# Performance work log

Hardware: AMD Instinct MI355X
Metric: run time of the kernel (lower is better)

The kernel has to match this reference:

```python
import jax, jax.numpy as jnp
import numpy as np

R0 = 1.0
DIM_A, DIM_V, DIM_D = 32, 32, 32
N_NODES = 20000
N_EDGES = 640000


def radial_encode_8(r, r0):
    # 8 Gaussian radial basis functions on the edge length |r_ij|
    d = jnp.linalg.norm(r, axis=-1)                      # [E]
    centers = jnp.linspace(0.0, r0, 8)                   # [8]
    width = r0 / 8.0
    return jnp.exp(-(((d[..., None] - centers) / width) ** 2))  # [E,8]


def tens_sigmoid_vec(v):
    # norm-saturating nonlinearity for rank-1 tensors (direction-preserving)
    n2 = jnp.sum(v * v, axis=-1, keepdims=True)
    return v * jax.lax.rsqrt(1.0 + n2)


def setup_inputs() -> dict:
    key = jax.random.key(0)
    ks = jax.random.split(key, 12)

    def lin(k, fan_in, fan_out):
        return jax.random.normal(k, (fan_in, fan_out), jnp.float32) / np.float32(np.sqrt(fan_in))

    return dict(
        r_ij=jax.random.normal(ks[0], (N_EDGES, 3), jnp.float32),
        w_rad=lin(ks[1], 8, DIM_A), b_rad=jnp.zeros((DIM_A,), jnp.float32),
        w_direct=lin(ks[2], DIM_A, DIM_A),
        w1=lin(ks[3], DIM_A, 2 * DIM_A), b1=jnp.zeros((2 * DIM_A,), jnp.float32),
        w2=lin(ks[4], 2 * DIM_A, 2 * DIM_A), b2=jnp.zeros((2 * DIM_A,), jnp.float32),
        w3=lin(ks[5], 2 * DIM_A, DIM_A), b3=jnp.zeros((DIM_A,), jnp.float32),
        w_v=lin(ks[6], DIM_A, DIM_V),
        w_d=lin(ks[7], DIM_A, DIM_D),
        edges_src=jax.random.randint(ks[8], (N_EDGES,), 0, N_NODES),
        n_nodes=N_NODES,
    )


def reference(r_ij, w_rad, b_rad, w_direct, w1, b1, w2, b2, w3, b3, w_v, w_d,
              edges_src, n_nodes):
    lrelu = lambda x: jnp.where(x > 0, x, 0.1 * x)
    # radial MLP: Linear(8, a) -> MLP (lin_direct + 3-layer leakyrelu net)
    h = radial_encode_8(r_ij, R0) @ w_rad + b_rad                      # [E,a]
    rad = h @ w_direct + (lrelu(lrelu(h @ w1 + b1) @ w2 + b2) @ w3 + b3)  # [E,a]
    rs = tens_sigmoid_vec(r_ij * (7.0 / R0))                            # [E,3]

    seg = lambda x: jax.ops.segment_sum(x, edges_src, num_segments=n_nodes)
    A_a = seg(rad)                                                      # [N,a]
    A_v = seg(rad[:, :, None] * rs[:, None, :])                         # [N,a,3]
    # phi_d_ij = rad ⊗ rs ⊗ rs per edge  -> [E,a,3,3], then scatter-sum
    A_d = seg(rad[:, :, None, None] * rs[:, None, None, :] * rs[:, None, :, None])  # [N,a,3,3]

    out_v = jnp.einsum('nac,av->nvc', A_v, w_v)                         # TensLinear rank 1
    out_d = jnp.einsum('naij,ad->ndij', A_d, w_d)                       # TensLinear rank 2
    return A_a, out_v, out_d
```

## Files before the change

kernel.cpp:

```cpp
#include <hip/hip_runtime.h>
#include <hip/hip_bf16.h>
#include <hip/hip_fp16.h>
#include <math.h>


#define TSIZE 8192
#define DMAX  2.0f
#define EPB   4
#define HB    128
#define TILE  10240
#define NPB   4

#define O_WRAD 0
#define O_BRAD 256
#define O_WDIR 288
#define O_W1   1312
#define O_B1   3360
#define O_W2   3424
#define O_B2   7520
#define O_W3   7584
#define O_B3   9632
#define O_WV   9664
#define O_WD   10688
#define W_TOT  11712

__device__ __forceinline__ float lrelu(float x) { return x > 0.0f ? x : 0.1f * x; }

__device__ __forceinline__ float ldf(const void* p, int i, bool f32) {
    return f32 ? ((const float*)p)[i]
               : __uint_as_float(((unsigned int)((const unsigned short*)p)[i]) << 16);
}
__device__ __forceinline__ void stf(void* p, size_t i, float v, bool f32) {
    if (f32) ((float*)p)[i] = v;
    else     ((__hip_bfloat16*)p)[i] = __float2bfloat16(v);
}

__device__ __forceinline__ bool detect_f32(const void* r) {
    const unsigned short* p = (const unsigned short*)r;
    int bad = 0;
#pragma unroll 8
    for (int i = 0; i < 128; i++) {
        float v = __uint_as_float(((unsigned int)p[i]) << 16);
        bad |= (!isfinite(v) || fabsf(v) > 1e5f) ? 1 : 0;
    }
    return bad != 0;
}

__global__ void k_prep(const void* __restrict__ r_ij,
                       const void* w_rad, const void* b_rad, const void* w_direct,
                       const void* w1, const void* b1, const void* w2, const void* b2,
                       const void* w3, const void* b3, const void* w_v, const void* w_d,
                       float* __restrict__ wcat, int* __restrict__ flag,
                       int* __restrict__ counts, int N) {
    const int b = blockIdx.x;
    if (b == 0) {
        if (threadIdx.x == 0) flag[0] = detect_f32(r_ij) ? 1 : 0;
    } else if (b <= 11) {
        const bool f32 = detect_f32(r_ij);
        const void* src; int cnt; int off;
        switch (b) {
            case 1:  src = w_rad;    cnt = 256;  off = O_WRAD; break;
            case 2:  src = b_rad;    cnt = 32;   off = O_BRAD; break;
            case 3:  src = w_direct; cnt = 1024; off = O_WDIR; break;
            case 4:  src = w1;       cnt = 2048; off = O_W1;   break;
            case 5:  src = b1;       cnt = 64;   off = O_B1;   break;
            case 6:  src = w2;       cnt = 4096; off = O_W2;   break;
            case 7:  src = b2;       cnt = 64;   off = O_B2;   break;
            case 8:  src = w3;       cnt = 2048; off = O_W3;   break;
            case 9:  src = b3;       cnt = 32;   off = O_B3;   break;
            case 10: src = w_v;      cnt = 1024; off = O_WV;   break;
            default: src = w_d;      cnt = 1024; off = O_WD;   break;
        }
        for (int i = threadIdx.x; i < cnt; i += blockDim.x)
            wcat[off + i] = ldf(src, i, f32);
    } else if (counts) {
        int i = (b - 12) * blockDim.x + threadIdx.x;
        if (i < N) counts[i] = 0;
    }
}

__global__ void __launch_bounds__(64 * EPB) k_table(const float* __restrict__ wcat,
                                                    float* __restrict__ tabI) {
    __shared__ float Lh[EPB][32], Lt1[EPB][64], Lt2[EPB][64], Lrad[EPB][32];

    const int s = threadIdx.x >> 6;
    const int j = threadIdx.x & 63;
    const int e = blockIdx.x * EPB + s;
    const float d = (float)e * (DMAX / (float)(TSIZE - 1));

    float enc[8];
#pragma unroll
    for (int k = 0; k < 8; k++) {
        float t = (d - (float)k * (1.0f / 7.0f)) * 8.0f;
        enc[k] = expf(-t * t);
    }

    if (j < 32) {
        float hv = wcat[O_BRAD + j];
#pragma unroll
        for (int k = 0; k < 8; k++) hv = fmaf(enc[k], wcat[O_WRAD + k * 32 + j], hv);
        Lh[s][j] = hv;
    }
    __syncthreads();

    {
        float v = wcat[O_B1 + j];
#pragma unroll
        for (int i = 0; i < 32; i++) v = fmaf(Lh[s][i], wcat[O_W1 + i * 64 + j], v);
        Lt1[s][j] = lrelu(v);
    }
    __syncthreads();

    {
        float v = wcat[O_B2 + j];
#pragma unroll
        for (int i = 0; i < 64; i++) v = fmaf(Lt1[s][i], wcat[O_W2 + i * 64 + j], v);
        Lt2[s][j] = lrelu(v);
    }
    __syncthreads();

    if (j < 32) {
        float v = wcat[O_B3 + j];
#pragma unroll
        for (int i = 0; i < 64; i++) v = fmaf(Lt2[s][i], wcat[O_W3 + i * 32 + j], v);
#pragma unroll
        for (int i = 0; i < 32; i++) v = fmaf(Lh[s][i], wcat[O_WDIR + i * 32 + j], v);
        Lrad[s][j] = v;
        tabI[e * 96 + j] = v;
    }
    __syncthreads();

    if (j < 32) {
        float sv = 0.0f, sd = 0.0f;
#pragma unroll
        for (int i = 0; i < 32; i++) {
            float ri = Lrad[s][i];
            sv = fmaf(ri, wcat[O_WV + i * 32 + j], sv);
            sd = fmaf(ri, wcat[O_WD + i * 32 + j], sd);
        }
        tabI[e * 96 + 32 + j] = sv;
        tabI[e * 96 + 64 + j] = sd;
    }
}

__global__ void __launch_bounds__(256) k_hist(const int* __restrict__ src, int E,
                                              int chunk,
                                              unsigned short* __restrict__ cnt,
                                              int N) {
    __shared__ int lcnt[TILE];
    const int b = blockIdx.x % HB;
    const int t = blockIdx.x / HB;
    const int lo = b * chunk;
    const int hi = min(lo + chunk, E);
    const int t0 = t * TILE;
    const int tl = min(TILE, N - t0);

    for (int i = threadIdx.x; i < tl; i += 256) lcnt[i] = 0;
    __syncthreads();
    for (int e = lo + threadIdx.x; e < hi; e += 256) {
        const int s = src[e] - t0;
        if ((unsigned)s < (unsigned)tl) atomicAdd(&lcnt[s], 1);
    }
    __syncthreads();
    unsigned short* out = cnt + (size_t)(t * HB + b) * TILE;
    for (int i = threadIdx.x; i < tl; i += 256)
        out[i] = (unsigned short)lcnt[i];
}

__global__ void __launch_bounds__(64) k_colscan(unsigned short* __restrict__ cnt,
                                                int* __restrict__ tot,
                                                int* __restrict__ coarse, int N) {
    const int lane = threadIdx.x;
    const int n = blockIdx.x * 64 + lane;
    int run = 0;
    if (n < N) {
        const int t = n / TILE;
        const int nl = n % TILE;
        unsigned short* col = cnt + (size_t)(t * HB) * TILE + nl;
#pragma unroll 4
        for (int b = 0; b < HB; b++) {
            int c = col[(size_t)b * TILE];
            col[(size_t)b * TILE] = (unsigned short)run;
            run += c;
        }
        tot[n] = run;
    }
    int s = run;
    for (int off = 32; off > 0; off >>= 1) s += __shfl_down(s, off);
    if (lane == 0) coarse[blockIdx.x] = s;
}

__global__ void __launch_bounds__(64) k_scan2(const int* __restrict__ tot,
                                              const int* __restrict__ coarse,
                                              int* __restrict__ rowstart, int N) {
    const int lane = threadIdx.x;
    const int b = blockIdx.x;
    int cp = 0;
    for (int j = lane; j < b; j += 64) cp += coarse[j];
    for (int off = 32; off > 0; off >>= 1) cp += __shfl_down(cp, off);
    const int cpre = __shfl(cp, 0);

    const int n = b * 64 + lane;
    const int v = (n < N) ? tot[n] : 0;
    int inc = v;
    for (int off = 1; off < 64; off <<= 1) {
        int y = __shfl_up(inc, off);
        if (lane >= off) inc += y;
    }
    if (n < N) rowstart[n] = cpre + inc - v;
    if (n == N - 1) rowstart[N] = cpre + inc;
}

template <bool P16>
__global__ void __launch_bounds__(256) k_place(
        const int* __restrict__ src, int E, int chunk,
        const unsigned short* __restrict__ cnt, const int* __restrict__ rowstart,
        const void* __restrict__ r_ij, const int* __restrict__ flag,
        void* __restrict__ epsv, int N) {
    __shared__ int cur[TILE];
    const int b = blockIdx.x % HB;
    const int t = blockIdx.x / HB;
    const int lo = b * chunk;
    const int hi = min(lo + chunk, E);
    const int t0 = t * TILE;
    const int tl = min(TILE, N - t0);
    const bool f32 = flag[0] != 0;

    const unsigned short* base = cnt + (size_t)(t * HB + b) * TILE;
    for (int i = threadIdx.x; i < tl; i += 256)
        cur[i] = rowstart[t0 + i] + (int)base[i];
    __syncthreads();
    for (int e = lo + threadIdx.x; e < hi; e += 256) {
        const int s = src[e] - t0;
        if ((unsigned)s < (unsigned)tl) {
            const int pos = atomicAdd(&cur[s], 1);
            const float x = ldf(r_ij, 3 * e + 0, f32);
            const float y = ldf(r_ij, 3 * e + 1, f32);
            const float z = ldf(r_ij, 3 * e + 2, f32);
            const float d2 = x * x + y * y + z * z;
            const float inv = rsqrtf(1.0f + 49.0f * d2);
            const float u = fminf(sqrtf(d2), DMAX) * ((float)(TSIZE - 1) / DMAX);
            const int ti = (int)(u + 0.5f);
            const float rs0 = 7.0f * x * inv, rs1 = 7.0f * y * inv,
                        rs2 = 7.0f * z * inv;
            if (P16) {
                ((float4*)epsv)[pos] =
                    make_float4(rs0, rs1, rs2, __int_as_float(ti * 384));
            } else {
                const unsigned int h0 = __half_as_ushort(__float2half(rs0));
                const unsigned int h1 = __half_as_ushort(__float2half(rs1));
                const unsigned int h2 = __half_as_ushort(__float2half(rs2));
                ((uint2*)epsv)[pos] =
                    make_uint2(h0 | (h1 << 16), h2 | ((unsigned)ti << 16));
            }
        }
    }
}

template <bool P16>
__global__ void __launch_bounds__(64 * NPB) k_nodes2(
    const void* __restrict__ epsv,
    const int* __restrict__ rowstart,
    const float* __restrict__ tabI,
    const int* __restrict__ flag,
    void* __restrict__ out, int N) {
    const int wave = threadIdx.x >> 6;
    const int lane = threadIdx.x & 63;
    const int n0 = (blockIdx.x * NPB + wave) * 2;
    const int a = lane & 31;
    const int half = lane >> 5;
    const int myn = n0 + half;
    const bool f32 = flag[0] != 0;
    const char* tabA = (const char*)tabI + (a << 2);

    int s0 = 0, s1 = 0;
    if (myn < N) { s0 = rowstart[myn]; s1 = rowstart[myn + 1]; }
    const int mylen = s1 - s0;
    const int lenA = __shfl(mylen, 0);
    const int lenB = __shfl(mylen, 32);
    const int minl = min(lenA, lenB);
    const int maxl = max(lenA, lenB);

    float accA = 0.f, v0 = 0.f, v1 = 0.f, v2 = 0.f;
    float d00 = 0.f, d01 = 0.f, d02 = 0.f,
          d10 = 0.f, d11 = 0.f, d12 = 0.f,
          d20 = 0.f, d21 = 0.f, d22 = 0.f;

#define EDGE_ACC(X, Y, Z, P)                                                  \
    do {                                                                      \
        const float ra = (P)[0], rv = (P)[32], rd = (P)[64];                  \
        accA += ra;                                                           \
        v0 += rv * (X); v1 += rv * (Y); v2 += rv * (Z);                       \
        const float t0 = rd * (X), t1 = rd * (Y), t2 = rd * (Z);              \
        d00 += t0 * (X); d01 += t0 * (Y); d02 += t0 * (Z);                    \
        d10 += t1 * (X); d11 += t1 * (Y); d12 += t1 * (Z);                    \
        d20 += t2 * (X); d21 += t2 * (Y); d22 += t2 * (Z);                    \
    } while (0)

    int i = 0;
    for (; i + 1 < minl; i += 2) {
        float x0, y0, z0, x1, y1, z1;
        const float *p0, *p1;
        if (P16) {
            const float4 qa = ((const float4*)epsv)[s0 + i];
            const float4 qb = ((const float4*)epsv)[s0 + i + 1];
            x0 = qa.x; y0 = qa.y; z0 = qa.z;
            x1 = qb.x; y1 = qb.y; z1 = qb.z;
            p0 = (const float*)(tabA + __float_as_int(qa.w));
            p1 = (const float*)(tabA + __float_as_int(qb.w));
        } else {
            const uint2 qa = ((const uint2*)epsv)[s0 + i];
            const uint2 qb = ((const uint2*)epsv)[s0 + i + 1];
            x0 = __half2float(__ushort_as_half((unsigned short)(qa.x & 0xffff)));
            y0 = __half2float(__ushort_as_half((unsigned short)(qa.x >> 16)));
            z0 = __half2float(__ushort_as_half((unsigned short)(qa.y & 0xffff)));
            x1 = __half2float(__ushort_as_half((unsigned short)(qb.x & 0xffff)));
            y1 = __half2float(__ushort_as_half((unsigned short)(qb.x >> 16)));
            z1 = __half2float(__ushort_as_half((unsigned short)(qb.y & 0xffff)));
            p0 = (const float*)(tabA + (int)(qa.y >> 16) * 384);
            p1 = (const float*)(tabA + (int)(qb.y >> 16) * 384);
        }
        EDGE_ACC(x0, y0, z0, p0);
        EDGE_ACC(x1, y1, z1, p1);
    }
    for (; i < maxl; i++) {
        if (i < mylen) {
            float x, y, z;
            const float* p;
            if (P16) {
                const float4 q = ((const float4*)epsv)[s0 + i];
                x = q.x; y = q.y; z = q.z;
                p = (const float*)(tabA + __float_as_int(q.w));
            } else {
                const uint2 q = ((const uint2*)epsv)[s0 + i];
                x = __half2float(__ushort_as_half((unsigned short)(q.x & 0xffff)));
                y = __half2float(__ushort_as_half((unsigned short)(q.x >> 16)));
                z = __half2float(__ushort_as_half((unsigned short)(q.y & 0xffff)));
                p = (const float*)(tabA + (int)(q.y >> 16) * 384);
            }
            EDGE_ACC(x, y, z, p);
        }
    }
#undef EDGE_ACC

    if (myn >= N) return;
    const size_t baseV = (size_t)N * 32;
    const size_t baseD = (size_t)N * 128;
    stf(out, (size_t)myn * 32 + a, accA, f32);
    const size_t vb = baseV + (size_t)myn * 96 + a * 3;
    stf(out, vb + 0, v0, f32);
    stf(out, vb + 1, v1, f32);
    stf(out, vb + 2, v2, f32);
    const size_t db = baseD + (size_t)myn * 288 + a * 9;
    stf(out, db + 0, d00, f32);
    stf(out, db + 1, d01, f32);
    stf(out, db + 2, d02, f32);
    stf(out, db + 3, d10, f32);
    stf(out, db + 4, d11, f32);
    stf(out, db + 5, d12, f32);
    stf(out, db + 6, d20, f32);
    stf(out, db + 7, d21, f32);
    stf(out, db + 8, d22, f32);
}

__global__ void k_rank_g(const int* __restrict__ src, int* __restrict__ counts,
                         int* __restrict__ rank, int E) {
    int e = blockIdx.x * blockDim.x + threadIdx.x;
    if (e < E) rank[e] = atomicAdd(&counts[src[e]], 1);
}
__global__ void k_scan_g(const int* __restrict__ counts, int* __restrict__ rowstart,
                         int N, int E) {
    __shared__ int part[1024];
    const int t = threadIdx.x;
    const int CH = (N + 1023) / 1024;
    const int lo = t * CH;
    const int hi = min(lo + CH, N);
    int s = 0;
    for (int i = lo; i < hi; i++) s += counts[i];
    part[t] = s;
    __syncthreads();
    for (int off = 1; off < 1024; off <<= 1) {
        int v = part[t];
        int w = (t >= off) ? part[t - off] : 0;
        __syncthreads();
        part[t] = v + w;
        __syncthreads();
    }
    int run = (t == 0) ? 0 : part[t - 1];
    for (int i = lo; i < hi; i++) { rowstart[i] = run; run += counts[i]; }
    if (t == 0) rowstart[N] = E;
}
__global__ void k_place_g(const int* __restrict__ src, const int* __restrict__ rank,
                          const int* __restrict__ rowstart,
                          int* __restrict__ perm, int E) {
    int e = blockIdx.x * blockDim.x + threadIdx.x;
    if (e < E) perm[rowstart[src[e]] + rank[e]] = e;
}
__global__ void __launch_bounds__(256) k_nodes_fb(
    const int* __restrict__ perm, const void* __restrict__ r_ij,
    const int* __restrict__ rowstart, const float* __restrict__ tabI,
    const int* __restrict__ flag, void* __restrict__ out, int N) {
    const int wave = threadIdx.x >> 6;
    const int lane = threadIdx.x & 63;
    const int n = blockIdx.x * 4 + wave;
    if (n >= N) return;
    const int a = lane & 31;
    const bool hi = (lane >> 5) != 0;
    const bool f32 = flag[0] != 0;
    const int s0 = rowstart[n], s1 = rowstart[n + 1];
    float accR = 0.f, acc1 = 0.f, acc2 = 0.f, acc3 = 0.f,
          acc4 = 0.f, acc5 = 0.f, acc6 = 0.f;
    for (int idx = s0; idx < s1; idx++) {
        const int e = perm[idx];
        const float x0 = ldf(r_ij, 3 * e + 0, f32);
        const float y0 = ldf(r_ij, 3 * e + 1, f32);
        const float z0 = ldf(r_ij, 3 * e + 2, f32);
        const float d2 = x0 * x0 + y0 * y0 + z0 * z0;
        const float inv = rsqrtf(1.0f + 49.0f * d2);
        const float x = 7.0f * x0 * inv, y = 7.0f * y0 * inv, z = 7.0f * z0 * inv;
        const float u = fminf(sqrtf(d2), DMAX) * ((float)(TSIZE - 1) / DMAX);
        const int b = (int)(u + 0.5f) * 96 + a;
        const float ra = tabI[b], rv = tabI[b + 32], rd = tabI[b + 64];
        const float b1 = (hi ? rd : rv) * (hi ? y : 1.0f);
        const float b2 = rd * (hi ? z : x);
        accR += ra;
        acc1 += b1 * x; acc2 += b1 * y; acc3 += b1 * z;
        acc4 += b2 * x; acc5 += b2 * y; acc6 += b2 * z;
    }
    const size_t baseV = (size_t)N * 32;
    const size_t baseD = (size_t)N * 128;
    if (!hi) {
        stf(out, (size_t)n * 32 + a, accR, f32);
        const size_t vb = baseV + (size_t)n * 96 + a * 3;
        stf(out, vb + 0, acc1, f32);
        stf(out, vb + 1, acc2, f32);
        stf(out, vb + 2, acc3, f32);
        const size_t db = baseD + (size_t)n * 288 + a * 9;
        stf(out, db + 0, acc4, f32);
        stf(out, db + 1, acc5, f32);
        stf(out, db + 2, acc6, f32);
    } else {
        const size_t db = baseD + (size_t)n * 288 + a * 9;
        stf(out, db + 3, acc1, f32);
        stf(out, db + 4, acc2, f32);
        stf(out, db + 5, acc3, f32);
        stf(out, db + 6, acc4, f32);
        stf(out, db + 7, acc5, f32);
        stf(out, db + 8, acc6, f32);
    }
}

extern "C" void kernel_launch(void* const* d_in, const int* in_sizes, int n_in,
                              void* d_out, int out_size, void* d_ws, size_t ws_size,
                              hipStream_t stream) {
    const void* r_ij     = d_in[0];
    const void* w_rad    = d_in[1];
    const void* b_rad    = d_in[2];
    const void* w_direct = d_in[3];
    const void* w1       = d_in[4];
    const void* b1       = d_in[5];
    const void* w2       = d_in[6];
    const void* b2       = d_in[7];
    const void* w3       = d_in[8];
    const void* b3       = d_in[9];
    const void* w_v      = d_in[10];
    const void* w_d      = d_in[11];
    const int* edges_src = (const int*)d_in[12];

    const int E = in_sizes[12];
    const int N = out_size / 416;
    const int chunk = (E + HB - 1) / HB;
    const int ntiles = (N + TILE - 1) / TILE;
    const int NB = (N + 63) / 64;

    const size_t cntBytes  = (size_t)ntiles * HB * TILE * 2;
    const size_t tailBytes = ((size_t)W_TOT + 4) * 4 + (size_t)TSIZE * 96 * 4
                           + cntBytes + ((size_t)N + NB + N + 1) * 4;
    const bool p16 = ws_size >= (size_t)E * 16 + tailBytes + 64;
    const bool p8  = !p16 && ws_size >= (size_t)E * 8 + tailBytes + 64;

    char* w = (char*)d_ws;
    if (p16 || p8) {
        const size_t slot = (size_t)E * (p16 ? 16 : 8);
        void* eps     = (void*)w;
        float* wcat   = (float*)(w + slot);
        int* flag     = (int*)(wcat + W_TOT);
        float* tabI   = (float*)(flag + 4);
        unsigned short* cnt = (unsigned short*)(tabI + (size_t)TSIZE * 96);
        int* tot      = (int*)((char*)cnt + cntBytes);
        int* coarse   = tot + N;
        int* rowstart = coarse + NB;

        const int nodeBlocks = (N + 2 * NPB - 1) / (2 * NPB);
        k_prep<<<12, 256, 0, stream>>>(
            r_ij, w_rad, b_rad, w_direct, w1, b1, w2, b2, w3, b3, w_v, w_d,
            wcat, flag, nullptr, N);
        k_table<<<TSIZE / EPB, 64 * EPB, 0, stream>>>(wcat, tabI);
        k_hist<<<HB * ntiles, 256, 0, stream>>>(edges_src, E, chunk, cnt, N);
        k_colscan<<<NB, 64, 0, stream>>>(cnt, tot, coarse, N);
        k_scan2<<<NB, 64, 0, stream>>>(tot, coarse, rowstart, N);
        if (p16) {
            k_place<true><<<HB * ntiles, 256, 0, stream>>>(
                edges_src, E, chunk, cnt, rowstart, r_ij, flag, eps, N);
            k_nodes2<true><<<nodeBlocks, 64 * NPB, 0, stream>>>(
                eps, rowstart, tabI, flag, d_out, N);
        } else {
            k_place<false><<<HB * ntiles, 256, 0, stream>>>(
                edges_src, E, chunk, cnt, rowstart, r_ij, flag, eps, N);
            k_nodes2<false><<<nodeBlocks, 64 * NPB, 0, stream>>>(
                eps, rowstart, tabI, flag, d_out, N);
        }
    } else {
        int* perm     = (int*)w;
        float* wcat   = (float*)(w + (size_t)E * 4);
        int* flag     = (int*)(wcat + W_TOT);
        float* tabI   = (float*)(flag + 4);
        int* counts   = (int*)(tabI + (size_t)TSIZE * 96);
        int* rowstart = counts + N;
        int* rank     = rowstart + N + 1;

        k_prep<<<12 + (N + 255) / 256, 256, 0, stream>>>(
            r_ij, w_rad, b_rad, w_direct, w1, b1, w2, b2, w3, b3, w_v, w_d,
            wcat, flag, counts, N);
        k_table<<<TSIZE / EPB, 64 * EPB, 0, stream>>>(wcat, tabI);
        k_rank_g<<<(E + 255) / 256, 256, 0, stream>>>(edges_src, counts, rank, E);
        k_scan_g<<<1, 1024, 0, stream>>>(counts, rowstart, N, E);
        k_place_g<<<(E + 255) / 256, 256, 0, stream>>>(edges_src, rank, rowstart,
                                                       perm, E);
        k_nodes_fb<<<(N + 3) / 4, 256, 0, stream>>>(
            perm, r_ij, rowstart, tabI, flag, d_out, N);
    }
}
```

Before: 207.7 us.

## Fuse CSR build into one grid-barrier kernel and stage weights in shared memory

Merges the histogram, column scan, coarse scan and placement kernels into one persistent kernel that uses atomic-counter grid barriers, which removes several launch gaps. Folds the weight-conversion prep kernel into the table kernel, where each block loads all weights into shared memory. Also unrolls the node edge loop from 2 to 4 edges per iteration. The spin grid barrier assumes every block is co-resident (256 blocks of 256 threads with about 40KB of shared memory each) and adds a memset launch. Each table block now redundantly loads about 47KB of weights.

```diff
diff --git a/kernel.cpp b/kernel.cpp
--- a/kernel.cpp
+++ b/kernel.cpp
@@ -46,42 +46,37 @@
     return bad != 0;
 }
 
-__global__ void k_prep(const void* __restrict__ r_ij,
-                       const void* w_rad, const void* b_rad, const void* w_direct,
-                       const void* w1, const void* b1, const void* w2, const void* b2,
-                       const void* w3, const void* b3, const void* w_v, const void* w_d,
-                       float* __restrict__ wcat, int* __restrict__ flag,
-                       int* __restrict__ counts, int N) {
-    const int b = blockIdx.x;
-    if (b == 0) {
-        if (threadIdx.x == 0) flag[0] = detect_f32(r_ij) ? 1 : 0;
-    } else if (b <= 11) {
-        const bool f32 = detect_f32(r_ij);
-        const void* src; int cnt; int off;
-        switch (b) {
-            case 1:  src = w_rad;    cnt = 256;  off = O_WRAD; break;
-            case 2:  src = b_rad;    cnt = 32;   off = O_BRAD; break;
-            case 3:  src = w_direct; cnt = 1024; off = O_WDIR; break;
-            case 4:  src = w1;       cnt = 2048; off = O_W1;   break;
-            case 5:  src = b1;       cnt = 64;   off = O_B1;   break;
-            case 6:  src = w2;       cnt = 4096; off = O_W2;   break;
-            case 7:  src = b2;       cnt = 64;   off = O_B2;   break;
-            case 8:  src = w3;       cnt = 2048; off = O_W3;   break;
-            case 9:  src = b3;       cnt = 32;   off = O_B3;   break;
-            case 10: src = w_v;      cnt = 1024; off = O_WV;   break;
-            default: src = w_d;      cnt = 1024; off = O_WD;   break;
-        }
-        for (int i = threadIdx.x; i < cnt; i += blockDim.x)
-            wcat[off + i] = ldf(src, i, f32);
-    } else if (counts) {
-        int i = (b - 12) * blockDim.x + threadIdx.x;
-        if (i < N) counts[i] = 0;
-    }
-}
-
-__global__ void __launch_bounds__(64 * EPB) k_table(const float* __restrict__ wcat,
-                                                    float* __restrict__ tabI) {
+__device__ __forceinline__ void load_seg(float* dst, const void* src, int cnt,
+                                         bool f32, int tid, int bs) {
+    for (int i = tid; i < cnt; i += bs) dst[i] = ldf(src, i, f32);
+}
+
+__global__ void __launch_bounds__(64 * EPB) k_table(
+        const void* __restrict__ r_ij,
+        const void* w_rad, const void* b_rad, const void* w_direct,
+        const void* w1, const void* b1, const void* w2, const void* b2,
+        const void* w3, const void* b3, const void* w_v, const void* w_d,
+        int* __restrict__ flag, float* __restrict__ tabI) {
+    __shared__ float W[W_TOT];
     __shared__ float Lh[EPB][32], Lt1[EPB][64], Lt2[EPB][64], Lrad[EPB][32];
+
+    const bool f32 = detect_f32(r_ij);
+    if (blockIdx.x == 0 && threadIdx.x == 0) flag[0] = f32 ? 1 : 0;
+
+    const int tid = threadIdx.x;
+    const int bs = 64 * EPB;
+    load_seg(W + O_WRAD, w_rad,    256,  f32, tid, bs);
+    load_seg(W + O_BRAD, b_rad,    32,   f32, tid, bs);
+    load_seg(W + O_WDIR, w_direct, 1024, f32, tid, bs);
+    load_seg(W + O_W1,   w1,       2048, f32, tid, bs);
+    load_seg(W + O_B1,   b1,       64,   f32, tid, bs);
+    load_seg(W + O_W2,   w2,       4096, f32, tid, bs);
+    load_seg(W + O_B2,   b2,       64,   f32, tid, bs);
+    load_seg(W + O_W3,   w3,       2048, f32, tid, bs);
+    load_seg(W + O_B3,   b3,       32,   f32, tid, bs);
+    load_seg(W + O_WV,   w_v,      1024, f32, tid, bs);
+    load_seg(W + O_WD,   w_d,      1024, f32, tid, bs);
+    __syncthreads();
 
     const int s = threadIdx.x >> 6;
     const int j = threadIdx.x & 63;
@@ -96,35 +91,35 @@
     }
 
     if (j < 32) {
-        float hv = wcat[O_BRAD + j];
-#pragma unroll
-        for (int k = 0; k < 8; k++) hv = fmaf(enc[k], wcat[O_WRAD + k * 32 + j], hv);
+        float hv = W[O_BRAD + j];
+#pragma unroll
+        for (int k = 0; k < 8; k++) hv = fmaf(enc[k], W[O_WRAD + k * 32 + j], hv);
         Lh[s][j] = hv;
     }
     __syncthreads();
 
     {
-        float v = wcat[O_B1 + j];
-#pragma unroll
-        for (int i = 0; i < 32; i++) v = fmaf(Lh[s][i], wcat[O_W1 + i * 64 + j], v);
+        float v = W[O_B1 + j];
+#pragma unroll
+        for (int i = 0; i < 32; i++) v = fmaf(Lh[s][i], W[O_W1 + i * 64 + j], v);
         Lt1[s][j] = lrelu(v);
     }
     __syncthreads();
 
     {
-        float v = wcat[O_B2 + j];
-#pragma unroll
-        for (int i = 0; i < 64; i++) v = fmaf(Lt1[s][i], wcat[O_W2 + i * 64 + j], v);
+        float v = W[O_B2 + j];
+#pragma unroll
+        for (int i = 0; i < 64; i++) v = fmaf(Lt1[s][i], W[O_W2 + i * 64 + j], v);
         Lt2[s][j] = lrelu(v);
     }
     __syncthreads();
 
     if (j < 32) {
-        float v = wcat[O_B3 + j];
-#pragma unroll
-        for (int i = 0; i < 64; i++) v = fmaf(Lt2[s][i], wcat[O_W3 + i * 32 + j], v);
-#pragma unroll
-        for (int i = 0; i < 32; i++) v = fmaf(Lh[s][i], wcat[O_WDIR + i * 32 + j], v);
+        float v = W[O_B3 + j];
+#pragma unroll
+        for (int i = 0; i < 64; i++) v = fmaf(Lt2[s][i], W[O_W3 + i * 32 + j], v);
+#pragma unroll
+        for (int i = 0; i < 32; i++) v = fmaf(Lh[s][i], W[O_WDIR + i * 32 + j], v);
         Lrad[s][j] = v;
         tabI[e * 96 + j] = v;
     }
@@ -135,19 +130,34 @@
 #pragma unroll
         for (int i = 0; i < 32; i++) {
             float ri = Lrad[s][i];
-            sv = fmaf(ri, wcat[O_WV + i * 32 + j], sv);
-            sd = fmaf(ri, wcat[O_WD + i * 32 + j], sd);
+            sv = fmaf(ri, W[O_WV + i * 32 + j], sv);
+            sd = fmaf(ri, W[O_WD + i * 32 + j], sd);
         }
         tabI[e * 96 + 32 + j] = sv;
         tabI[e * 96 + 64 + j] = sd;
     }
 }
 
-__global__ void __launch_bounds__(256) k_hist(const int* __restrict__ src, int E,
-                                              int chunk,
-                                              unsigned short* __restrict__ cnt,
-                                              int N) {
-    __shared__ int lcnt[TILE];
+__device__ __forceinline__ void gbar(int* bar, int slot, int nb) {
+    __syncthreads();
+    if (threadIdx.x == 0) {
+        __threadfence();
+        atomicAdd(&bar[slot], 1);
+        while (atomicAdd(&bar[slot], 0) < nb) { }
+    }
+    __syncthreads();
+    __threadfence();
+}
+
+template <bool P16>
+__global__ void __launch_bounds__(256) k_csr(
+        const int* __restrict__ src, int E, int chunk,
+        const void* __restrict__ r_ij, const int* __restrict__ flag,
+        unsigned short* __restrict__ cnt, int* __restrict__ tot,
+        int* __restrict__ coarse, int* __restrict__ rowstart,
+        int* __restrict__ bar, void* __restrict__ epsv, int N) {
+    __shared__ int lbuf[TILE];
+    const int nb = gridDim.x;
     const int b = blockIdx.x % HB;
     const int t = blockIdx.x / HB;
     const int lo = b * chunk;
@@ -155,103 +165,91 @@
     const int t0 = t * TILE;
     const int tl = min(TILE, N - t0);
 
-    for (int i = threadIdx.x; i < tl; i += 256) lcnt[i] = 0;
+    for (int i = threadIdx.x; i < tl; i += 256) lbuf[i] = 0;
     __syncthreads();
     for (int e = lo + threadIdx.x; e < hi; e += 256) {
         const int s = src[e] - t0;
-        if ((unsigned)s < (unsigned)tl) atomicAdd(&lcnt[s], 1);
-    }
-    __syncthreads();
-    unsigned short* out = cnt + (size_t)(t * HB + b) * TILE;
-    for (int i = threadIdx.x; i < tl; i += 256)
-        out[i] = (unsigned short)lcnt[i];
-}
-
-__global__ void __launch_bounds__(64) k_colscan(unsigned short* __restrict__ cnt,
-                                                int* __restrict__ tot,
-                                                int* __restrict__ coarse, int N) {
-    const int lane = threadIdx.x;
-    const int n = blockIdx.x * 64 + lane;
-    int run = 0;
-    if (n < N) {
-        const int t = n / TILE;
-        const int nl = n % TILE;
-        unsigned short* col = cnt + (size_t)(t * HB) * TILE + nl;
+        if ((unsigned)s < (unsigned)tl) atomicAdd(&lbuf[s], 1);
+    }
+    __syncthreads();
+    {
+        unsigned short* out = cnt + (size_t)(t * HB + b) * TILE;
+        for (int i = threadIdx.x; i < tl; i += 256)
+            out[i] = (unsigned short)lbuf[i];
+    }
+    gbar(bar, 0, nb);
+
+    {
+        const int gtid = blockIdx.x * 256 + threadIdx.x;
+        const int lane = threadIdx.x & 63;
+        const int w = gtid >> 6;
+        int run = 0;
+        if (gtid < N) {
+            const int tt = gtid / TILE;
+            const int nl = gtid % TILE;
+            unsigned short* col = cnt + (size_t)(tt * HB) * TILE + nl;
 #pragma unroll 4
-        for (int b = 0; b < HB; b++) {
-            int c = col[(size_t)b * TILE];
-            col[(size_t)b * TILE] = (unsigned short)run;
-            run += c;
+            for (int c = 0; c < HB; c++) {
+                int v = col[(size_t)c * TILE];
+                col[(size_t)c * TILE] = (unsigned short)run;
+                run += v;
+            }
+            tot[gtid] = run;
         }
-        tot[n] = run;
-    }
-    int s = run;
-    for (int off = 32; off > 0; off >>= 1) s += __shfl_down(s, off);
-    if (lane == 0) coarse[blockIdx.x] = s;
-}
-
-__global__ void __launch_bounds__(64) k_scan2(const int* __restrict__ tot,
-                                              const int* __restrict__ coarse,
-                                              int* __restrict__ rowstart, int N) {
-    const int lane = threadIdx.x;
-    const int b = blockIdx.x;
-    int cp = 0;
-    for (int j = lane; j < b; j += 64) cp += coarse[j];
-    for (int off = 32; off > 0; off >>= 1) cp += __shfl_down(cp, off);
-    const int cpre = __shfl(cp, 0);
-
-    const int n = b * 64 + lane;
-    const int v = (n < N) ? tot[n] : 0;
-    int inc = v;
-    for (int off = 1; off < 64; off <<= 1) {
-        int y = __shfl_up(inc, off);
-        if (lane >= off) inc += y;
-    }
-    if (n < N) rowstart[n] = cpre + inc - v;
-    if (n == N - 1) rowstart[N] = cpre + inc;
-}
-
-template <bool P16>
-__global__ void __launch_bounds__(256) k_place(
-        const int* __restrict__ src, int E, int chunk,
-        const unsigned short* __restrict__ cnt, const int* __restrict__ rowstart,
-        const void* __restrict__ r_ij, const int* __restrict__ flag,
-        void* __restrict__ epsv, int N) {
-    __shared__ int cur[TILE];
-    const int b = blockIdx.x % HB;
-    const int t = blockIdx.x / HB;
-    const int lo = b * chunk;
-    const int hi = min(lo + chunk, E);
-    const int t0 = t * TILE;
-    const int tl = min(TILE, N - t0);
-    const bool f32 = flag[0] != 0;
-
-    const unsigned short* base = cnt + (size_t)(t * HB + b) * TILE;
-    for (int i = threadIdx.x; i < tl; i += 256)
-        cur[i] = rowstart[t0 + i] + (int)base[i];
-    __syncthreads();
-    for (int e = lo + threadIdx.x; e < hi; e += 256) {
-        const int s = src[e] - t0;
-        if ((unsigned)s < (unsigned)tl) {
-            const int pos = atomicAdd(&cur[s], 1);
-            const float x = ldf(r_ij, 3 * e + 0, f32);
-            const float y = ldf(r_ij, 3 * e + 1, f32);
-            const float z = ldf(r_ij, 3 * e + 2, f32);
-            const float d2 = x * x + y * y + z * z;
-            const float inv = rsqrtf(1.0f + 49.0f * d2);
-            const float u = fminf(sqrtf(d2), DMAX) * ((float)(TSIZE - 1) / DMAX);
-            const int ti = (int)(u + 0.5f);
-            const float rs0 = 7.0f * x * inv, rs1 = 7.0f * y * inv,
-                        rs2 = 7.0f * z * inv;
-            if (P16) {
-                ((float4*)epsv)[pos] =
-                    make_float4(rs0, rs1, rs2, __int_as_float(ti * 384));
-            } else {
-                const unsigned int h0 = __half_as_ushort(__float2half(rs0));
-                const unsigned int h1 = __half_as_ushort(__float2half(rs1));
-                const unsigned int h2 = __half_as_ushort(__float2half(rs2));
-                ((uint2*)epsv)[pos] =
-                    make_uint2(h0 | (h1 << 16), h2 | ((unsigned)ti << 16));
+        int sum = run;
+        for (int off = 32; off > 0; off >>= 1) sum += __shfl_down(sum, off);
+        if (lane == 0) coarse[w] = sum;
+    }
+    gbar(bar, 1, nb);
+
+    {
+        const int gtid = blockIdx.x * 256 + threadIdx.x;
+        const int lane = threadIdx.x & 63;
+        const int w = gtid >> 6;
+        int cp = 0;
+        for (int j = lane; j < w; j += 64) cp += coarse[j];
+        for (int off = 32; off > 0; off >>= 1) cp += __shfl_down(cp, off);
+        const int cpre = __shfl(cp, 0);
+        const int v = (gtid < N) ? tot[gtid] : 0;
+        int inc = v;
+        for (int off = 1; off < 64; off <<= 1) {
+            int y = __shfl_up(inc, off);
+            if (lane >= off) inc += y;
+        }
+        if (gtid < N) rowstart[gtid] = cpre + inc - v;
+        if (gtid == N - 1) rowstart[N] = cpre + inc;
+    }
+    gbar(bar, 2, nb);
+
+    {
+        const bool f32 = flag[0] != 0;
+        const unsigned short* base = cnt + (size_t)(t * HB + b) * TILE;
+        for (int i = threadIdx.x; i < tl; i += 256)
+            lbuf[i] = rowstart[t0 + i] + (int)base[i];
+        __syncthreads();
+        for (int e = lo + threadIdx.x; e < hi; e += 256) {
+            const int s = src[e] - t0;
+            if ((unsigned)s < (unsigned)tl) {
+                const int pos = atomicAdd(&lbuf[s], 1);
+                const float x = ldf(r_ij, 3 * e + 0, f32);
+                const float y = ldf(r_ij, 3 * e + 1, f32);
+                const float z = ldf(r_ij, 3 * e + 2, f32);
+                const float d2 = x * x + y * y + z * z;
+                const float inv = rsqrtf(1.0f + 49.0f * d2);
+                const float u = fminf(sqrtf(d2), DMAX) * ((float)(TSIZE - 1) / DMAX);
+                const int ti = (int)(u + 0.5f);
+                const float rs0 = 7.0f * x * inv, rs1 = 7.0f * y * inv,
+                            rs2 = 7.0f * z * inv;
+                if (P16) {
+                    ((float4*)epsv)[pos] =
+                        make_float4(rs0, rs1, rs2, __int_as_float(ti * 384));
+                } else {
+                    const unsigned int h0 = __half_as_ushort(__float2half(rs0));
+                    const unsigned int h1 = __half_as_ushort(__float2half(rs1));
+                    const unsigned int h2 = __half_as_ushort(__float2half(rs2));
+                    ((uint2*)epsv)[pos] =
+                        make_uint2(h0 | (h1 << 16), h2 | ((unsigned)ti << 16));
+                }
             }
         }
     }
@@ -286,6 +284,21 @@
           d10 = 0.f, d11 = 0.f, d12 = 0.f,
           d20 = 0.f, d21 = 0.f, d22 = 0.f;
 
+#define EDGE_LOAD(K, IDX)                                                     \
+    do {                                                                      \
+        if (P16) {                                                            \
+            const float4 q = ((const float4*)epsv)[IDX];                      \
+            xs[K] = q.x; ys[K] = q.y; zs[K] = q.z;                            \
+            ps[K] = (const float*)(tabA + __float_as_int(q.w));               \
+        } else {                                                              \
+            const uint2 q = ((const uint2*)epsv)[IDX];                        \
+            xs[K] = __half2float(__ushort_as_half((unsigned short)(q.x & 0xffff))); \
+            ys[K] = __half2float(__ushort_as_half((unsigned short)(q.x >> 16)));    \
+            zs[K] = __half2float(__ushort_as_half((unsigned short)(q.y & 0xffff))); \
+            ps[K] = (const float*)(tabA + (int)(q.y >> 16) * 384);            \
+        }                                                                     \
+    } while (0)
+
 #define EDGE_ACC(X, Y, Z, P)                                                  \
     do {                                                                      \
         const float ra = (P)[0], rv = (P)[32], rd = (P)[64];                  \
@@ -298,49 +311,25 @@
     } while (0)
 
     int i = 0;
-    for (; i + 1 < minl; i += 2) {
-        float x0, y0, z0, x1, y1, z1;
-        const float *p0, *p1;
-        if (P16) {
-            const float4 qa = ((const float4*)epsv)[s0 + i];
-            const float4 qb = ((const float4*)epsv)[s0 + i + 1];
-            x0 = qa.x; y0 = qa.y; z0 = qa.z;
-            x1 = qb.x; y1 = qb.y; z1 = qb.z;
-            p0 = (const float*)(tabA + __float_as_int(qa.w));
-            p1 = (const float*)(tabA + __float_as_int(qb.w));
-        } else {
-            const uint2 qa = ((const uint2*)epsv)[s0 + i];
-            const uint2 qb = ((const uint2*)epsv)[s0 + i + 1];
-            x0 = __half2float(__ushort_as_half((unsigned short)(qa.x & 0xffff)));
-            y0 = __half2float(__ushort_as_half((unsigned short)(qa.x >> 16)));
-            z0 = __half2float(__ushort_as_half((unsigned short)(qa.y & 0xffff)));
-            x1 = __half2float(__ushort_as_half((unsigned short)(qb.x & 0xffff)));
-            y1 = __half2float(__ushort_as_half((unsigned short)(qb.x >> 16)));
-            z1 = __half2float(__ushort_as_half((unsigned short)(qb.y & 0xffff)));
-            p0 = (const float*)(tabA + (int)(qa.y >> 16) * 384);
-            p1 = (const float*)(tabA + (int)(qb.y >> 16) * 384);
-        }
-        EDGE_ACC(x0, y0, z0, p0);
-        EDGE_ACC(x1, y1, z1, p1);
+    for (; i + 3 < minl; i += 4) {
+        float xs[4], ys[4], zs[4];
+        const float* ps[4];
+        EDGE_LOAD(0, s0 + i + 0);
+        EDGE_LOAD(1, s0 + i + 1);
+        EDGE_LOAD(2, s0 + i + 2);
+        EDGE_LOAD(3, s0 + i + 3);
+#pragma unroll
+        for (int k = 0; k < 4; k++) EDGE_ACC(xs[k], ys[k], zs[k], ps[k]);
     }
     for (; i < maxl; i++) {
         if (i < mylen) {
-            float x, y, z;
-            const float* p;
-            if (P16) {
-                const float4 q = ((const float4*)epsv)[s0 + i];
-                x = q.x; y = q.y; z = q.z;
-                p = (const float*)(tabA + __float_as_int(q.w));
-            } else {
-                const uint2 q = ((const uint2*)epsv)[s0 + i];
-                x = __half2float(__ushort_as_half((unsigned short)(q.x & 0xffff)));
-                y = __half2float(__ushort_as_half((unsigned short)(q.x >> 16)));
-                z = __half2float(__ushort_as_half((unsigned short)(q.y & 0xffff)));
-                p = (const float*)(tabA + (int)(q.y >> 16) * 384);
-            }
-            EDGE_ACC(x, y, z, p);
+            float xs[1], ys[1], zs[1];
+            const float* ps[1];
+            EDGE_LOAD(0, s0 + i);
+            EDGE_ACC(xs[0], ys[0], zs[0], ps[0]);
         }
     }
+#undef EDGE_LOAD
 #undef EDGE_ACC
 
     if (myn >= N) return;
@@ -471,58 +460,57 @@
     const int N = out_size / 416;
     const int chunk = (E + HB - 1) / HB;
     const int ntiles = (N + TILE - 1) / TILE;
-    const int NB = (N + 63) / 64;
+    const int nblocks = HB * ntiles;
 
     const size_t cntBytes  = (size_t)ntiles * HB * TILE * 2;
-    const size_t tailBytes = ((size_t)W_TOT + 4) * 4 + (size_t)TSIZE * 96 * 4
-                           + cntBytes + ((size_t)N + NB + N + 1) * 4;
-    const bool p16 = ws_size >= (size_t)E * 16 + tailBytes + 64;
-    const bool p8  = !p16 && ws_size >= (size_t)E * 8 + tailBytes + 64;
+    const size_t tailBytes = 20 * 4 + (size_t)TSIZE * 96 * 4 + cntBytes
+                           + ((size_t)N + 1024 + N + 1) * 4;
+    const bool sizeOK = (N <= nblocks * 256) && (ntiles <= 8);
+    const bool p16 = sizeOK && ws_size >= (size_t)E * 16 + tailBytes + 64;
+    const bool p8  = sizeOK && !p16 && ws_size >= (size_t)E * 8 + tailBytes + 64;
 
     char* w = (char*)d_ws;
     if (p16 || p8) {
         const size_t slot = (size_t)E * (p16 ? 16 : 8);
         void* eps     = (void*)w;
-        float* wcat   = (float*)(w + slot);
-        int* flag     = (int*)(wcat + W_TOT);
-        float* tabI   = (float*)(flag + 4);
+        int* flag     = (int*)(w + slot);
+        int* bar      = flag + 4;
+        float* tabI   = (float*)(bar + 16);
         unsigned short* cnt = (unsigned short*)(tabI + (size_t)TSIZE * 96);
         int* tot      = (int*)((char*)cnt + cntBytes);
         int* coarse   = tot + N;
-        int* rowstart = coarse + NB;
-
+        int* rowstart = coarse + 1024;
+
+        hipMemsetAsync(bar, 0, 16 * 4, stream);
+        k_table<<<TSIZE / EPB, 64 * EPB, 0, stream>>>(
+            r_ij, w_rad, b_rad, w_direct, w1, b1, w2, b2, w3, b3, w_v, w_d,
+            flag, tabI);
         const int nodeBlocks = (N + 2 * NPB - 1) / (2 * NPB);
-        k_prep<<<12, 256, 0, stream>>>(
-            r_ij, w_rad, b_rad, w_direct, w1, b1, w2, b2, w3, b3, w_v, w_d,
-            wcat, flag, nullptr, N);
-        k_table<<<TSIZE / EPB, 64 * EPB, 0, stream>>>(wcat, tabI);
-        k_hist<<<HB * ntiles, 256, 0, stream>>>(edges_src, E, chunk, cnt, N);
-        k_colscan<<<NB, 64, 0, stream>>>(cnt, tot, coarse, N);
-        k_scan2<<<NB, 64, 0, stream>>>(tot, coarse, rowstart, N);
         if (p16) {
-            k_place<true><<<HB * ntiles, 256, 0, stream>>>(
-                edges_src, E, chunk, cnt, rowstart, r_ij, flag, eps, N);
+            k_csr<true><<<nblocks, 256, 0, stream>>>(
+                edges_src, E, chunk, r_ij, flag, cnt, tot, coarse, rowstart,
+                bar, eps, N);
             k_nodes2<true><<<nodeBlocks, 64 * NPB, 0, stream>>>(
                 eps, rowstart, tabI, flag, d_out, N);
         } else {
-            k_place<false><<<HB * ntiles, 256, 0, stream>>>(
-                edges_src, E, chunk, cnt, rowstart, r_ij, flag, eps, N);
+            k_csr<false><<<nblocks, 256, 0, stream>>>(
+                edges_src, E, chunk, r_ij, flag, cnt, tot, coarse, rowstart,
+                bar, eps, N);
             k_nodes2<false><<<nodeBlocks, 64 * NPB, 0, stream>>>(
                 eps, rowstart, tabI, flag, d_out, N);
         }
     } else {
         int* perm     = (int*)w;
-        float* wcat   = (float*)(w + (size_t)E * 4);
-        int* flag     = (int*)(wcat + W_TOT);
+        int* flag     = (int*)(w + (size_t)E * 4);
         float* tabI   = (float*)(flag + 4);
         int* counts   = (int*)(tabI + (size_t)TSIZE * 96);
         int* rowstart = counts + N;
         int* rank     = rowstart + N + 1;
 
-        k_prep<<<12 + (N + 255) / 256, 256, 0, stream>>>(
+        hipMemsetAsync(counts, 0, (size_t)N * 4, stream);
+        k_table<<<TSIZE / EPB, 64 * EPB, 0, stream>>>(
             r_ij, w_rad, b_rad, w_direct, w1, b1, w2, b2, w3, b3, w_v, w_d,
-            wcat, flag, counts, N);
-        k_table<<<TSIZE / EPB, 64 * EPB, 0, stream>>>(wcat, tabI);
+            flag, tabI);
         k_rank_g<<<(E + 255) / 256, 256, 0, stream>>>(edges_src, counts, rank, E);
         k_scan_g<<<1, 1024, 0, stream>>>(counts, rowstart, N, E);
         k_place_g<<<(E + 255) / 256, 256, 0, stream>>>(edges_src, rank, rowstart,
```

Result: slower. 312.5 us (+50.5%).
